# Optimization experiments

Hardware: AMD Instinct MI355X
Metric: run time of the kernel (lower is better)

The kernel has to match this reference:

```python
import jax, jax.numpy as jnp
import numpy as np

T, B, VD, KD, HD, OD = 64, 256, 64, 64, 512, 4


def setup_inputs() -> dict:
    key = jax.random.key(0)
    ks = jax.random.split(key, 20)
    s = 0.05
    p = {}
    p["images"] = jax.random.normal(ks[0], (T, B, 3, 32, 32), jnp.float32)
    # encoder: Conv(3->32,k4,s2) ReLU Conv(32->64,k4,s2) ReLU Conv(64->64,k4,s2) Flatten Linear(256->VD)
    p["conv1_w"] = jax.random.normal(ks[1], (32, 3, 4, 4), jnp.float32) * s
    p["conv1_b"] = jnp.zeros((32,), jnp.float32)
    p["conv2_w"] = jax.random.normal(ks[2], (64, 32, 4, 4), jnp.float32) * s
    p["conv2_b"] = jnp.zeros((64,), jnp.float32)
    p["conv3_w"] = jax.random.normal(ks[3], (64, 64, 4, 4), jnp.float32) * s
    p["conv3_b"] = jnp.zeros((64,), jnp.float32)
    p["enc_w"] = jax.random.normal(ks[4], (VD, 256), jnp.float32) * s
    p["enc_b"] = jnp.zeros((VD,), jnp.float32)
    # LSTMCell(key_dim+1 -> hidden_dim), torch gate order i,f,g,o
    p["w_ih"] = jax.random.normal(ks[5], (4 * HD, KD + 1), jnp.float32) * s
    p["w_hh"] = jax.random.normal(ks[6], (4 * HD, HD), jnp.float32) * s
    p["b_ih"] = jnp.zeros((4 * HD,), jnp.float32)
    p["b_hh"] = jnp.zeros((4 * HD,), jnp.float32)
    p["out_w"] = jax.random.normal(ks[7], (OD, HD), jnp.float32) * s
    p["out_b"] = jnp.zeros((OD,), jnp.float32)
    p["gate_w"] = jax.random.normal(ks[8], (1, HD), jnp.float32) * s
    p["gate_b"] = jnp.zeros((1,), jnp.float32)
    p["key_w"] = jax.random.normal(ks[9], (KD, HD), jnp.float32) * s
    p["key_b"] = jnp.zeros((KD,), jnp.float32)
    p["conf_w"] = jax.random.normal(ks[10], (1, 1), jnp.float32)
    p["conf_b"] = jnp.zeros((1,), jnp.float32)
    return p


def reference(images, conv1_w, conv1_b, conv2_w, conv2_b, conv3_w, conv3_b,
              enc_w, enc_b, w_ih, w_hh, b_ih, b_hh, out_w, out_b,
              gate_w, gate_b, key_w, key_b, conf_w, conf_b):
    Tn, Bn = images.shape[0], images.shape[1]

    def conv(x, w, b, relu):
        y = jax.lax.conv_general_dilated(
            x, w, window_strides=(2, 2), padding='VALID',
            dimension_numbers=('NCHW', 'OIHW', 'NCHW'))
        y = y + b[None, :, None, None]
        return jax.nn.relu(y) if relu else y

    # Encode all timesteps at once (same math as per-step encoder calls).
    x = images.reshape((Tn * Bn, 3, 32, 32))
    x = conv(x, conv1_w, conv1_b, True)
    x = conv(x, conv2_w, conv2_b, True)
    x = conv(x, conv3_w, conv3_b, False)  # no ReLU after 3rd conv in Sequential
    z_all = (x.reshape((Tn * Bn, -1)) @ enc_w.T + enc_b).reshape((Tn, Bn, -1))

    def lstm(x, h, c):
        g = x @ w_ih.T + b_ih + h @ w_hh.T + b_hh
        i, f, gg, o = jnp.split(g, 4, axis=-1)
        c2 = jax.nn.sigmoid(f) * c + jax.nn.sigmoid(i) * jnp.tanh(gg)
        return jax.nn.sigmoid(o) * jnp.tanh(c2), c2

    HDn = w_hh.shape[1]
    KDn = key_w.shape[0]
    VDn = z_all.shape[-1]
    slots = jnp.arange(Tn)

    def step(carry, xs):
        hx, cx, kx, Mk, Mv = carry
        z, t = xs
        hx, cx = lstm(kx, hx, cx)
        y = hx @ out_w.T + out_b
        g = hx @ gate_w.T + gate_b          # (b,1)
        kw = hx @ key_w.T + key_b           # (b,KD)
        # content-addressed read over the (masked) growing memory
        sim = jnp.einsum('bnd,bd->bn', Mv, z)
        mask = (slots < t)[None, :]
        wk = jax.nn.softmax(jnp.where(mask, sim, -1e30), axis=-1)
        ck = jax.nn.sigmoid(sim[..., None] * conf_w[0, 0] + conf_b[0])  # (b,n,1)
        mem = jnp.concatenate([Mk, ck], axis=-1)                         # (b,n,KD+1)
        kx_att = jax.nn.sigmoid(g) * jnp.einsum('bn,bnd->bd', wk, mem)
        kx_new = jnp.where(t == 0, jnp.zeros_like(kx_att), kx_att)      # k0 at first step
        # gated write: append kw / z at slot t
        Mk = Mk.at[:, t, :].set(kw)
        Mv = Mv.at[:, t, :].set(z)
        return (hx, cx, kx_new, Mk, Mv), y

    init = (jnp.zeros((Bn, HDn), images.dtype),
            jnp.zeros((Bn, HDn), images.dtype),
            jnp.zeros((Bn, KDn + 1), images.dtype),
            jnp.zeros((Bn, Tn, KDn), images.dtype),
            jnp.zeros((Bn, Tn, VDn), images.dtype))
    _, ys = jax.lax.scan(step, init, (z_all, slots))
    return ys  # (T, B, output_dim)
```

## Files before the change

kernel.cpp:

```cpp
#include <hip/hip_runtime.h>
#include <math.h>


__device__ __forceinline__ float sigm(float x) { return 1.0f / (1.0f + expf(-x)); }

#define PREP_N (1187840 + 2048 + 1536 + 32768 + 65536 + 16384)
__global__ __launch_bounds__(256) void prep_kernel(
    const float* __restrict__ w_ih, const float* __restrict__ w_hh,
    const float* __restrict__ b_ih, const float* __restrict__ b_hh,
    const float* __restrict__ w1, const float* __restrict__ w2,
    const float* __restrict__ w3, const float* __restrict__ ew,
    float* __restrict__ WT, float* __restrict__ bsum,
    float* __restrict__ w1T, float* __restrict__ w2T,
    float* __restrict__ w3T, float* __restrict__ ewT)
{
  int i = blockIdx.x * 256 + threadIdx.x;
  if (i < 1187840) {
    const int r = i >> 11, c = i & 2047;
    float v;
    if (r < 65)       v = w_ih[(size_t)c * 65 + r];
    else if (r < 577) v = w_hh[(size_t)c * 512 + (r - 65)];
    else              v = 0.0f;
    WT[i] = v; return;
  }
  i -= 1187840;
  if (i < 2048) { bsum[i] = b_ih[i] + b_hh[i]; return; }
  i -= 2048;
  if (i < 1536) { const int r = i >> 5, oc = i & 31; w1T[i] = w1[oc * 48 + r]; return; }
  i -= 1536;
  if (i < 32768) { const int r = i >> 6, oc = i & 63; w2T[i] = w2[oc * 512 + r]; return; }
  i -= 32768;
  if (i < 65536) { const int r = i >> 6, oc = i & 63; w3T[i] = w3[oc * 1024 + r]; return; }
  i -= 65536;
  if (i < 16384) { const int k = i >> 6, d = i & 63; ewT[i] = ew[d * 256 + k]; return; }
}

#define ENT 192
__global__ __launch_bounds__(ENT) void encoder_kernel(
    const float* __restrict__ images,
    const float* __restrict__ w1T, const float* __restrict__ b1,
    const float* __restrict__ w2T, const float* __restrict__ b2,
    const float* __restrict__ w3T, const float* __restrict__ b3,
    const float* __restrict__ ewT, const float* __restrict__ eb,
    float* __restrict__ z_all)
{
  __shared__ __align__(16) float c1[7744];
  __shared__ __align__(16) float buf[3072];
  const int bid = blockIdx.x;
  const int tid = threadIdx.x;

  {
    const float4* src = (const float4*)(images + (size_t)bid * 3072);
    float4* dst = (float4*)buf;
    for (int i = tid; i < 768; i += ENT) dst[i] = src[i];
  }
  __syncthreads();

  for (int s = tid; s < 360; s += ENT) {
    const int ocg  = s & 7;
    const int pg   = s >> 3;
    const int row  = pg / 3;
    const int colg = pg - row * 3;
    const int ox0  = colg * 5;
    float acc[4][5];
    #pragma unroll
    for (int o = 0; o < 4; ++o) {
      const float bb = b1[ocg * 4 + o];
      #pragma unroll
      for (int p = 0; p < 5; ++p) acc[o][p] = bb;
    }
    #pragma unroll
    for (int ic = 0; ic < 3; ++ic) {
      #pragma unroll
      for (int ky = 0; ky < 4; ++ky) {
        const int y = 2 * row + ky;
        const float* ib = &buf[ic * 1024 + y * 32 + 2 * ox0];
        float v[12];
        #pragma unroll
        for (int i = 0; i < 6; ++i) { float2 t2 = *(const float2*)(ib + 2 * i); v[2*i] = t2.x; v[2*i+1] = t2.y; }
        float w_[4][4];
        #pragma unroll
        for (int kx = 0; kx < 4; ++kx)
          *(float4*)&w_[kx][0] = *(const float4*)(w1T + (ic * 16 + ky * 4 + kx) * 32 + ocg * 4);
        #pragma unroll
        for (int o = 0; o < 4; ++o)
          #pragma unroll
          for (int p = 0; p < 5; ++p)
            acc[o][p] += w_[0][o] * v[2*p] + w_[1][o] * v[2*p+1] + w_[2][o] * v[2*p+2] + w_[3][o] * v[2*p+3];
      }
    }
    #pragma unroll
    for (int o = 0; o < 4; ++o)
      #pragma unroll
      for (int p = 0; p < 5; ++p)
        c1[(ocg * 4 + o) * 242 + row * 16 + ox0 + p] = fmaxf(acc[o][p], 0.0f);
  }
  __syncthreads();

  {
    const int ocg = tid & 15;
    const int pg  = tid >> 4;
    const int row = pg >> 1;
    const int ox0 = (pg & 1) * 3;
    float acc[4][3];
    #pragma unroll
    for (int o = 0; o < 4; ++o) {
      const float bb = b2[ocg * 4 + o];
      acc[o][0] = bb; acc[o][1] = bb; acc[o][2] = bb;
    }
    for (int ic = 0; ic < 32; ++ic) {
      #pragma unroll
      for (int ky = 0; ky < 4; ++ky) {
        const int y = 2 * row + ky;
        const float* ib = &c1[ic * 242 + y * 16 + 2 * ox0];
        float v[8];
        #pragma unroll
        for (int i = 0; i < 4; ++i) { float2 t2 = *(const float2*)(ib + 2 * i); v[2*i] = t2.x; v[2*i+1] = t2.y; }
        float w_[4][4];
        #pragma unroll
        for (int kx = 0; kx < 4; ++kx)
          *(float4*)&w_[kx][0] = *(const float4*)(w2T + (ic * 16 + ky * 4 + kx) * 64 + ocg * 4);
        #pragma unroll
        for (int o = 0; o < 4; ++o)
          #pragma unroll
          for (int p = 0; p < 3; ++p)
            acc[o][p] += w_[0][o] * v[2*p] + w_[1][o] * v[2*p+1] + w_[2][o] * v[2*p+2] + w_[3][o] * v[2*p+3];
      }
    }
    __syncthreads();
    #pragma unroll
    for (int o = 0; o < 4; ++o)
      #pragma unroll
      for (int p = 0; p < 3; ++p)
        buf[(ocg * 4 + o) * 38 + row * 6 + ox0 + p] = fmaxf(acc[o][p], 0.0f);
  }
  __syncthreads();

  {
    const int oc = tid & 63;
    const int kc = tid >> 6;
    const int k0 = (kc * 256) / 3, k1 = ((kc + 1) * 256) / 3;
    float acc[4] = {0.f, 0.f, 0.f, 0.f};
    for (int it = k0; it < k1; ++it) {
      const int ic = it >> 2;
      const int ky = it & 3;
      float v[2][6];
      #pragma unroll
      for (int oy = 0; oy < 2; ++oy) {
        const float* ib = &buf[ic * 38 + (2 * oy + ky) * 6];
        #pragma unroll
        for (int i = 0; i < 3; ++i) { float2 t2 = *(const float2*)(ib + 2 * i); v[oy][2*i] = t2.x; v[oy][2*i+1] = t2.y; }
      }
      float w_[4];
      #pragma unroll
      for (int kx = 0; kx < 4; ++kx) w_[kx] = w3T[(ic * 16 + ky * 4 + kx) * 64 + oc];
      #pragma unroll
      for (int p = 0; p < 4; ++p) {
        const int oy = p >> 1, ox = p & 1;
        acc[p] += w_[0] * v[oy][2*ox] + w_[1] * v[oy][2*ox+1] + w_[2] * v[oy][2*ox+2] + w_[3] * v[oy][2*ox+3];
      }
    }
    #pragma unroll
    for (int p = 0; p < 4; ++p) c1[kc * 260 + p * 64 + oc] = acc[p];
  }
  __syncthreads();

  for (int o = tid; o < 256; o += ENT) {
    const int oc = o >> 2, p = o & 3;
    c1[1024 + o] = b3[oc] + c1[p * 64 + oc] + c1[260 + p * 64 + oc] + c1[520 + p * 64 + oc];
  }
  __syncthreads();

  {
    const int d  = tid & 63;
    const int kc = tid >> 6;
    const int k0 = (kc * 256) / 3, k1 = ((kc + 1) * 256) / 3;
    float s = 0.0f;
    for (int k = k0; k < k1; ++k) s += ewT[k * 64 + d] * c1[1024 + k];
    c1[1536 + kc * 64 + d] = s;
  }
  __syncthreads();
  if (tid < 64) {
    z_all[(size_t)bid * 64 + tid] = eb[tid] + c1[1536 + tid] + c1[1600 + tid] + c1[1664 + tid];
  }
}

__global__ __launch_bounds__(256) void gram_kernel(
    const float* __restrict__ z_all, float* __restrict__ z_gram)
{
  const int b = blockIdx.x;
  const int tid = threadIdx.x;
  __shared__ float zsb[64 * 65];
  for (int i = tid; i < 4096; i += 256) {
    const int tt = i >> 6, d = i & 63;
    zsb[tt * 65 + d] = z_all[((size_t)tt * 256 + b) * 64 + d];
  }
  __syncthreads();
  const int n = tid & 63, tg = tid >> 6;
  for (int tt = tg; tt < 64; tt += 4) {
    float s = 0.0f;
    #pragma unroll
    for (int d = 0; d < 64; ++d) s += zsb[tt * 65 + d] * zsb[n * 65 + d];
    z_gram[((size_t)b * 64 + tt) * 64 + n] = s;
  }
}

__global__ __launch_bounds__(256) void gates_partial_kernel(
    const float* __restrict__ XC, const float* __restrict__ WT,
    float* __restrict__ Gp, const int kchunk, const int klog)
{
  extern __shared__ float xs[];
  const int bx  = blockIdx.x;
  const int kc  = bx & ((1 << klog) - 1);
  const int jt  = bx >> klog;
  const int tid = threadIdx.x;
  const int tj  = tid & 63, tb = tid >> 6;
  const int k0  = kc * kchunk;
  const int b0  = blockIdx.y * 16;
  const int j0  = jt * 256 + tj * 4;

  const int NS = 16 * kchunk;
  for (int i = tid; i < NS; i += 256) {
    const int b = i / kchunk, k = i - b * kchunk;
    xs[b * kchunk + k] = XC[(size_t)(b0 + b) * 580 + k0 + k];
  }
  __syncthreads();

  float acc[4][4];
  #pragma unroll
  for (int bb = 0; bb < 4; ++bb)
    #pragma unroll
    for (int jj = 0; jj < 4; ++jj) acc[bb][jj] = 0.0f;

  const float* wp = WT + (size_t)k0 * 2048 + j0;
  const float* xp = xs + tb * 4 * kchunk;
  #pragma unroll 4
  for (int k = 0; k < kchunk; ++k) {
    const float4 w = *(const float4*)(wp + (size_t)k * 2048);
    #pragma unroll
    for (int bb = 0; bb < 4; ++bb) {
      const float xv = xp[bb * kchunk + k];
      acc[bb][0] += xv * w.x; acc[bb][1] += xv * w.y;
      acc[bb][2] += xv * w.z; acc[bb][3] += xv * w.w;
    }
  }
  #pragma unroll
  for (int bb = 0; bb < 4; ++bb) {
    float4 r; r.x = acc[bb][0]; r.y = acc[bb][1]; r.z = acc[bb][2]; r.w = acc[bb][3];
    *(float4*)(Gp + ((size_t)kc * 256 + b0 + tb * 4 + bb) * 2048 + j0) = r;
  }
}

__global__ __launch_bounds__(256) void step_fused_kernel(
    const int t, const int kcn,
    const float* __restrict__ Gp, const float* __restrict__ bsum,
    float* __restrict__ C, const float* __restrict__ z_gram,
    float* __restrict__ MkT, float* __restrict__ XC, float* __restrict__ out,
    const float* __restrict__ out_w, const float* __restrict__ out_b,
    const float* __restrict__ gate_w, const float* __restrict__ gate_b,
    const float* __restrict__ key_w, const float* __restrict__ key_b,
    const float* __restrict__ conf_w, const float* __restrict__ conf_b)
{
  const int b   = blockIdx.x;
  const int tid = threadIdx.x;
  __shared__ __align__(16) float hs[512];
  __shared__ __align__(16) float wks[64];
  __shared__ __align__(16) float psum[256];
  __shared__ float sgv, kx64v;

  for (int jj = tid; jj < 512; jj += 256) {
    float gv[4];
    #pragma unroll
    for (int g = 0; g < 4; ++g) {
      float s = bsum[g * 512 + jj];
      for (int kc = 0; kc < kcn; ++kc)
        s += Gp[((size_t)kc * 256 + b) * 2048 + g * 512 + jj];
      gv[g] = s;
    }
    const size_t cidx = (size_t)b * 512 + jj;
    const float c2v = sigm(gv[1]) * C[cidx] + sigm(gv[0]) * tanhf(gv[2]);
    C[cidx] = c2v;
    const float h = sigm(gv[3]) * tanhf(c2v);
    hs[jj] = h;
    XC[(size_t)b * 580 + 65 + jj] = h;
  }
  __syncthreads();

  const int wv = tid >> 6, lane = tid & 63;
  for (int d = wv; d < 69; d += 4) {
    const float* row = (d < 64) ? (key_w + (size_t)d * 512)
                     : (d < 68) ? (out_w + (size_t)(d - 64) * 512)
                                : gate_w;
    float a = 0.0f;
    #pragma unroll
    for (int k = 0; k < 8; ++k) a += hs[lane + k * 64] * row[lane + k * 64];
    #pragma unroll
    for (int m = 32; m > 0; m >>= 1) a += __shfl_xor(a, m);
    if (lane == 0) {
      if (d < 64)      MkT[(size_t)b * 4096 + d * 64 + t] = a + key_b[d];
      else if (d < 68) out[(size_t)t * 1024 + b * 4 + (d - 64)] = a + out_b[d - 64];
      else             sgv = sigm(a + gate_b[0]);
    }
  }
  __syncthreads();

  if (t == 0) {
    if (tid < 65) XC[(size_t)b * 580 + tid] = 0.0f;
    return;
  }

  if (tid < 64) {
    const int n = tid;
    const float sim = z_gram[((size_t)b * 64 + t) * 64 + n];
    const bool valid = (n < t);
    float mx = valid ? sim : -3.0e38f;
    #pragma unroll
    for (int m = 32; m > 0; m >>= 1) mx = fmaxf(mx, __shfl_xor(mx, m));
    const float p = valid ? expf(sim - mx) : 0.0f;
    float sum = p;
    #pragma unroll
    for (int m = 32; m > 0; m >>= 1) sum += __shfl_xor(sum, m);
    const float wk = p / sum;
    wks[n] = wk;
    float kc = wk * sigm(sim * conf_w[0] + conf_b[0]);
    #pragma unroll
    for (int m = 32; m > 0; m >>= 1) kc += __shfl_xor(kc, m);
    if (n == 0) kx64v = kc;
  }
  __syncthreads();

  {
    const int d = tid >> 2, q = tid & 3;
    const float* mr = MkT + (size_t)b * 4096 + d * 64 + q * 16;
    const float* wr = wks + q * 16;
    float a = 0.0f;
    #pragma unroll
    for (int i = 0; i < 4; ++i) {
      const float4 m4 = *(const float4*)(mr + 4 * i);
      const float4 w4 = *(const float4*)(wr + 4 * i);
      a += m4.x * w4.x + m4.y * w4.y + m4.z * w4.z + m4.w * w4.w;
    }
    psum[tid] = a;
  }
  __syncthreads();
  if (tid < 64) {
    XC[(size_t)b * 580 + tid] = sgv * (psum[tid * 4] + psum[tid * 4 + 1] + psum[tid * 4 + 2] + psum[tid * 4 + 3]);
  } else if (tid == 64) {
    XC[(size_t)b * 580 + 64] = sgv * kx64v;
  }
}

extern "C" void kernel_launch(void* const* d_in, const int* in_sizes, int n_in,
                              void* d_out, int out_size, void* d_ws, size_t ws_size,
                              hipStream_t stream) {
  const float* images = (const float*)d_in[0];
  const float* w1     = (const float*)d_in[1];
  const float* b1     = (const float*)d_in[2];
  const float* w2     = (const float*)d_in[3];
  const float* b2     = (const float*)d_in[4];
  const float* w3     = (const float*)d_in[5];
  const float* b3     = (const float*)d_in[6];
  const float* ew     = (const float*)d_in[7];
  const float* eb     = (const float*)d_in[8];
  const float* w_ih   = (const float*)d_in[9];
  const float* w_hh   = (const float*)d_in[10];
  const float* b_ih   = (const float*)d_in[11];
  const float* b_hh   = (const float*)d_in[12];
  const float* out_w  = (const float*)d_in[13];
  const float* out_b  = (const float*)d_in[14];
  const float* gate_w = (const float*)d_in[15];
  const float* gate_b = (const float*)d_in[16];
  const float* key_w  = (const float*)d_in[17];
  const float* key_b  = (const float*)d_in[18];
  const float* conf_w = (const float*)d_in[19];
  const float* conf_b = (const float*)d_in[20];
  float* out = (float*)d_out;
  float* ws  = (float*)d_ws;

  float* WT     = ws;
  float* bsum   = ws + 1187840;
  float* w1T    = ws + 1189888;
  float* w2T    = ws + 1191424;
  float* w3T    = ws + 1224192;
  float* ewT    = ws + 1289728;
  float* z_all  = ws + 1306112;
  float* MkT    = ws + 2354688;
  float* C      = ws + 3403264;
  float* XC     = ws + 3534336;
  float* z_gram = ws + 3682816;
  float* Gp     = ws + 4731392;

  int kcn = 4, klog = 2, kchunk = 145;
  if (ws_size < (4731392ull + 4ull * 524288ull) * 4ull) { kcn = 2; klog = 1; kchunk = 290; }
  if (ws_size < (4731392ull + 2ull * 524288ull) * 4ull) { kcn = 1; klog = 0; kchunk = 580; }

  hipMemsetAsync(C,  0, 131072 * sizeof(float), stream);
  hipMemsetAsync(XC, 0, 148480 * sizeof(float), stream);

  prep_kernel<<<(PREP_N + 255) / 256, 256, 0, stream>>>(
      w_ih, w_hh, b_ih, b_hh, w1, w2, w3, ew, WT, bsum, w1T, w2T, w3T, ewT);

  encoder_kernel<<<16384, ENT, 0, stream>>>(images, w1T, b1, w2T, b2, w3T, b3, ewT, eb, z_all);

  gram_kernel<<<256, 256, 0, stream>>>(z_all, z_gram);

  const size_t lds_stage = (size_t)16 * kchunk * sizeof(float);
  for (int t = 0; t < 64; ++t) {
    gates_partial_kernel<<<dim3(8 * kcn, 16), 256, lds_stage, stream>>>(
        XC, WT, Gp, kchunk, klog);
    step_fused_kernel<<<256, 256, 0, stream>>>(
        t, kcn, Gp, bsum, C, z_gram, MkT, XC, out,
        out_w, out_b, gate_w, gate_b, key_w, key_b, conf_w, conf_b);
  }
}
```

Before: 4.132 ms.

## Fuse recurrent scan into one cooperative kernel and split encoder conv1

The 64-step recurrence, which used two kernel launches per step, now runs as a single cooperative persistent kernel that uses grid-wide syncs between the gate GEMM phase and the per-batch update phase. When workspace allows, the encoder is also split into a conv1 kernel that writes its activations to global memory and a second kernel that runs the remaining layers. This targets per-step launch overhead and encoder occupancy, which the large LDS use of the fused encoder had limited. In exchange it adds grid.sync costs, global round trips for conv1 outputs, and depends on the cooperative grid fitting co-resident on the device.

```diff
diff --git a/kernel.cpp b/kernel.cpp
--- a/kernel.cpp
+++ b/kernel.cpp
@@ -1,5 +1,8 @@
 #include <hip/hip_runtime.h>
+#include <hip/hip_cooperative_groups.h>
 #include <math.h>
+
+namespace cg = cooperative_groups;
 
 
 __device__ __forceinline__ float sigm(float x) { return 1.0f / (1.0f + expf(-x)); }
@@ -36,6 +39,169 @@
 }
 
 #define ENT 192
+__global__ __launch_bounds__(ENT) void conv1_kernel(
+    const float* __restrict__ images,
+    const float* __restrict__ w1T, const float* __restrict__ b1,
+    float* __restrict__ c1g, const int s0)
+{
+  __shared__ __align__(16) float buf[3072];
+  const int bid = blockIdx.x;
+  const int tid = threadIdx.x;
+  {
+    const float4* src = (const float4*)(images + (size_t)(s0 + bid) * 3072);
+    float4* dst = (float4*)buf;
+    for (int i = tid; i < 768; i += ENT) dst[i] = src[i];
+  }
+  __syncthreads();
+
+  float* outp = c1g + (size_t)bid * 7680;
+  for (int s = tid; s < 360; s += ENT) {
+    const int ocg  = s & 7;
+    const int pg   = s >> 3;
+    const int row  = pg / 3;
+    const int colg = pg - row * 3;
+    const int ox0  = colg * 5;
+    float acc[4][5];
+    #pragma unroll
+    for (int o = 0; o < 4; ++o) {
+      const float bb = b1[ocg * 4 + o];
+      #pragma unroll
+      for (int p = 0; p < 5; ++p) acc[o][p] = bb;
+    }
+    #pragma unroll
+    for (int ic = 0; ic < 3; ++ic) {
+      #pragma unroll
+      for (int ky = 0; ky < 4; ++ky) {
+        const int y = 2 * row + ky;
+        const float* ib = &buf[ic * 1024 + y * 32 + 2 * ox0];
+        float v[12];
+        #pragma unroll
+        for (int i = 0; i < 6; ++i) { float2 t2 = *(const float2*)(ib + 2 * i); v[2*i] = t2.x; v[2*i+1] = t2.y; }
+        float w_[4][4];
+        #pragma unroll
+        for (int kx = 0; kx < 4; ++kx)
+          *(float4*)&w_[kx][0] = *(const float4*)(w1T + (ic * 16 + ky * 4 + kx) * 32 + ocg * 4);
+        #pragma unroll
+        for (int o = 0; o < 4; ++o)
+          #pragma unroll
+          for (int p = 0; p < 5; ++p)
+            acc[o][p] += w_[0][o] * v[2*p] + w_[1][o] * v[2*p+1] + w_[2][o] * v[2*p+2] + w_[3][o] * v[2*p+3];
+      }
+    }
+    #pragma unroll
+    for (int o = 0; o < 4; ++o)
+      #pragma unroll
+      for (int p = 0; p < 5; ++p)
+        outp[(ocg * 4 + o) * 240 + row * 16 + ox0 + p] = fmaxf(acc[o][p], 0.0f);
+  }
+}
+
+__global__ __launch_bounds__(ENT) void enc2_kernel(
+    const float* __restrict__ c1g,
+    const float* __restrict__ w2T, const float* __restrict__ b2,
+    const float* __restrict__ w3T, const float* __restrict__ b3,
+    const float* __restrict__ ewT, const float* __restrict__ eb,
+    float* __restrict__ z_all, const int s0)
+{
+  __shared__ __align__(16) float c1[7680];
+  __shared__ __align__(16) float buf[2432];
+  const int bid = blockIdx.x;
+  const int tid = threadIdx.x;
+
+  {
+    const float4* src = (const float4*)(c1g + (size_t)bid * 7680);
+    float4* dst = (float4*)c1;
+    for (int i = tid; i < 1920; i += ENT) dst[i] = src[i];
+  }
+  __syncthreads();
+
+  {
+    const int ocg = tid & 15;
+    const int pg  = tid >> 4;
+    const int row = pg >> 1;
+    const int ox0 = (pg & 1) * 3;
+    float acc[4][3];
+    #pragma unroll
+    for (int o = 0; o < 4; ++o) {
+      const float bb = b2[ocg * 4 + o];
+      acc[o][0] = bb; acc[o][1] = bb; acc[o][2] = bb;
+    }
+    for (int ic = 0; ic < 32; ++ic) {
+      #pragma unroll
+      for (int ky = 0; ky < 4; ++ky) {
+        const int y = 2 * row + ky;
+        const float* ib = &c1[ic * 240 + y * 16 + 2 * ox0];
+        float v[8];
+        #pragma unroll
+        for (int i = 0; i < 4; ++i) { float2 t2 = *(const float2*)(ib + 2 * i); v[2*i] = t2.x; v[2*i+1] = t2.y; }
+        float w_[4][4];
+        #pragma unroll
+        for (int kx = 0; kx < 4; ++kx)
+          *(float4*)&w_[kx][0] = *(const float4*)(w2T + (ic * 16 + ky * 4 + kx) * 64 + ocg * 4);
+        #pragma unroll
+        for (int o = 0; o < 4; ++o)
+          #pragma unroll
+          for (int p = 0; p < 3; ++p)
+            acc[o][p] += w_[0][o] * v[2*p] + w_[1][o] * v[2*p+1] + w_[2][o] * v[2*p+2] + w_[3][o] * v[2*p+3];
+      }
+    }
+    #pragma unroll
+    for (int o = 0; o < 4; ++o)
+      #pragma unroll
+      for (int p = 0; p < 3; ++p)
+        buf[(ocg * 4 + o) * 38 + row * 6 + ox0 + p] = fmaxf(acc[o][p], 0.0f);
+  }
+  __syncthreads();
+
+  {
+    const int oc = tid & 63;
+    const int kc = tid >> 6;
+    const int k0 = (kc * 256) / 3, k1 = ((kc + 1) * 256) / 3;
+    float acc[4] = {0.f, 0.f, 0.f, 0.f};
+    for (int it = k0; it < k1; ++it) {
+      const int ic = it >> 2;
+      const int ky = it & 3;
+      float v[2][6];
+      #pragma unroll
+      for (int oy = 0; oy < 2; ++oy) {
+        const float* ib = &buf[ic * 38 + (2 * oy + ky) * 6];
+        #pragma unroll
+        for (int i = 0; i < 3; ++i) { float2 t2 = *(const float2*)(ib + 2 * i); v[oy][2*i] = t2.x; v[oy][2*i+1] = t2.y; }
+      }
+      float w_[4];
+      #pragma unroll
+      for (int kx = 0; kx < 4; ++kx) w_[kx] = w3T[(ic * 16 + ky * 4 + kx) * 64 + oc];
+      #pragma unroll
+      for (int p = 0; p < 4; ++p) {
+        const int oy = p >> 1, ox = p & 1;
+        acc[p] += w_[0] * v[oy][2*ox] + w_[1] * v[oy][2*ox+1] + w_[2] * v[oy][2*ox+2] + w_[3] * v[oy][2*ox+3];
+      }
+    }
+    #pragma unroll
+    for (int p = 0; p < 4; ++p) c1[kc * 260 + p * 64 + oc] = acc[p];
+  }
+  __syncthreads();
+
+  for (int o = tid; o < 256; o += ENT) {
+    const int oc = o >> 2, p = o & 3;
+    c1[1024 + o] = b3[oc] + c1[p * 64 + oc] + c1[260 + p * 64 + oc] + c1[520 + p * 64 + oc];
+  }
+  __syncthreads();
+
+  {
+    const int d  = tid & 63;
+    const int kc = tid >> 6;
+    const int k0 = (kc * 256) / 3, k1 = ((kc + 1) * 256) / 3;
+    float s = 0.0f;
+    for (int k = k0; k < k1; ++k) s += ewT[k * 64 + d] * c1[1024 + k];
+    c1[1536 + kc * 64 + d] = s;
+  }
+  __syncthreads();
+  if (tid < 64) {
+    z_all[(size_t)(s0 + bid) * 64 + tid] = eb[tid] + c1[1536 + tid] + c1[1600 + tid] + c1[1664 + tid];
+  }
+}
+
 __global__ __launch_bounds__(ENT) void encoder_kernel(
     const float* __restrict__ images,
     const float* __restrict__ w1T, const float* __restrict__ b1,
@@ -48,14 +214,12 @@
   __shared__ __align__(16) float buf[3072];
   const int bid = blockIdx.x;
   const int tid = threadIdx.x;
-
   {
     const float4* src = (const float4*)(images + (size_t)bid * 3072);
     float4* dst = (float4*)buf;
     for (int i = tid; i < 768; i += ENT) dst[i] = src[i];
   }
   __syncthreads();
-
   for (int s = tid; s < 360; s += ENT) {
     const int ocg  = s & 7;
     const int pg   = s >> 3;
@@ -96,7 +260,6 @@
         c1[(ocg * 4 + o) * 242 + row * 16 + ox0 + p] = fmaxf(acc[o][p], 0.0f);
   }
   __syncthreads();
-
   {
     const int ocg = tid & 15;
     const int pg  = tid >> 4;
@@ -135,7 +298,6 @@
         buf[(ocg * 4 + o) * 38 + row * 6 + ox0 + p] = fmaxf(acc[o][p], 0.0f);
   }
   __syncthreads();
-
   {
     const int oc = tid & 63;
     const int kc = tid >> 6;
@@ -164,13 +326,11 @@
     for (int p = 0; p < 4; ++p) c1[kc * 260 + p * 64 + oc] = acc[p];
   }
   __syncthreads();
-
   for (int o = tid; o < 256; o += ENT) {
     const int oc = o >> 2, p = o & 3;
     c1[1024 + o] = b3[oc] + c1[p * 64 + oc] + c1[260 + p * 64 + oc] + c1[520 + p * 64 + oc];
   }
   __syncthreads();
-
   {
     const int d  = tid & 63;
     const int kc = tid >> 6;
@@ -205,148 +365,148 @@
   }
 }
 
-__global__ __launch_bounds__(256) void gates_partial_kernel(
-    const float* __restrict__ XC, const float* __restrict__ WT,
-    float* __restrict__ Gp, const int kchunk, const int klog)
-{
-  extern __shared__ float xs[];
-  const int bx  = blockIdx.x;
-  const int kc  = bx & ((1 << klog) - 1);
-  const int jt  = bx >> klog;
-  const int tid = threadIdx.x;
-  const int tj  = tid & 63, tb = tid >> 6;
-  const int k0  = kc * kchunk;
-  const int b0  = blockIdx.y * 16;
-  const int j0  = jt * 256 + tj * 4;
-
-  const int NS = 16 * kchunk;
-  for (int i = tid; i < NS; i += 256) {
-    const int b = i / kchunk, k = i - b * kchunk;
-    xs[b * kchunk + k] = XC[(size_t)(b0 + b) * 580 + k0 + k];
-  }
-  __syncthreads();
-
-  float acc[4][4];
-  #pragma unroll
-  for (int bb = 0; bb < 4; ++bb)
-    #pragma unroll
-    for (int jj = 0; jj < 4; ++jj) acc[bb][jj] = 0.0f;
-
-  const float* wp = WT + (size_t)k0 * 2048 + j0;
-  const float* xp = xs + tb * 4 * kchunk;
-  #pragma unroll 4
-  for (int k = 0; k < kchunk; ++k) {
-    const float4 w = *(const float4*)(wp + (size_t)k * 2048);
-    #pragma unroll
-    for (int bb = 0; bb < 4; ++bb) {
-      const float xv = xp[bb * kchunk + k];
-      acc[bb][0] += xv * w.x; acc[bb][1] += xv * w.y;
-      acc[bb][2] += xv * w.z; acc[bb][3] += xv * w.w;
-    }
-  }
-  #pragma unroll
-  for (int bb = 0; bb < 4; ++bb) {
-    float4 r; r.x = acc[bb][0]; r.y = acc[bb][1]; r.z = acc[bb][2]; r.w = acc[bb][3];
-    *(float4*)(Gp + ((size_t)kc * 256 + b0 + tb * 4 + bb) * 2048 + j0) = r;
-  }
-}
-
-__global__ __launch_bounds__(256) void step_fused_kernel(
-    const int t, const int kcn,
-    const float* __restrict__ Gp, const float* __restrict__ bsum,
+__global__ __launch_bounds__(256, 2) void scan_coop_kernel(
+    const float* __restrict__ WT, const float* __restrict__ bsum,
     float* __restrict__ C, const float* __restrict__ z_gram,
-    float* __restrict__ MkT, float* __restrict__ XC, float* __restrict__ out,
+    float* __restrict__ MkT, float* __restrict__ XC, float* __restrict__ Gp,
+    float* __restrict__ o_ptr,
     const float* __restrict__ out_w, const float* __restrict__ out_b,
     const float* __restrict__ gate_w, const float* __restrict__ gate_b,
     const float* __restrict__ key_w, const float* __restrict__ key_b,
-    const float* __restrict__ conf_w, const float* __restrict__ conf_b)
+    const float* __restrict__ conf_w, const float* __restrict__ conf_b,
+    const int kcn, const int klog, const int kchunk)
 {
-  const int b   = blockIdx.x;
+  cg::grid_group grid = cg::this_grid();
+  __shared__ __align__(16) float smem[16 * 580];
+
   const int tid = threadIdx.x;
-  __shared__ __align__(16) float hs[512];
-  __shared__ __align__(16) float wks[64];
-  __shared__ __align__(16) float psum[256];
-  __shared__ float sgv, kx64v;
-
-  for (int jj = tid; jj < 512; jj += 256) {
-    float gv[4];
-    #pragma unroll
-    for (int g = 0; g < 4; ++g) {
-      float s = bsum[g * 512 + jj];
-      for (int kc = 0; kc < kcn; ++kc)
-        s += Gp[((size_t)kc * 256 + b) * 2048 + g * 512 + jj];
-      gv[g] = s;
-    }
-    const size_t cidx = (size_t)b * 512 + jj;
-    const float c2v = sigm(gv[1]) * C[cidx] + sigm(gv[0]) * tanhf(gv[2]);
-    C[cidx] = c2v;
-    const float h = sigm(gv[3]) * tanhf(c2v);
-    hs[jj] = h;
-    XC[(size_t)b * 580 + 65 + jj] = h;
-  }
-  __syncthreads();
-
-  const int wv = tid >> 6, lane = tid & 63;
-  for (int d = wv; d < 69; d += 4) {
-    const float* row = (d < 64) ? (key_w + (size_t)d * 512)
-                     : (d < 68) ? (out_w + (size_t)(d - 64) * 512)
-                                : gate_w;
-    float a = 0.0f;
-    #pragma unroll
-    for (int k = 0; k < 8; ++k) a += hs[lane + k * 64] * row[lane + k * 64];
-    #pragma unroll
-    for (int m = 32; m > 0; m >>= 1) a += __shfl_xor(a, m);
-    if (lane == 0) {
-      if (d < 64)      MkT[(size_t)b * 4096 + d * 64 + t] = a + key_b[d];
-      else if (d < 68) out[(size_t)t * 1024 + b * 4 + (d - 64)] = a + out_b[d - 64];
-      else             sgv = sigm(a + gate_b[0]);
-    }
-  }
-  __syncthreads();
-
-  if (t == 0) {
-    if (tid < 65) XC[(size_t)b * 580 + tid] = 0.0f;
-    return;
-  }
-
-  if (tid < 64) {
-    const int n = tid;
-    const float sim = z_gram[((size_t)b * 64 + t) * 64 + n];
-    const bool valid = (n < t);
-    float mx = valid ? sim : -3.0e38f;
-    #pragma unroll
-    for (int m = 32; m > 0; m >>= 1) mx = fmaxf(mx, __shfl_xor(mx, m));
-    const float p = valid ? expf(sim - mx) : 0.0f;
-    float sum = p;
-    #pragma unroll
-    for (int m = 32; m > 0; m >>= 1) sum += __shfl_xor(sum, m);
-    const float wk = p / sum;
-    wks[n] = wk;
-    float kc = wk * sigm(sim * conf_w[0] + conf_b[0]);
-    #pragma unroll
-    for (int m = 32; m > 0; m >>= 1) kc += __shfl_xor(kc, m);
-    if (n == 0) kx64v = kc;
-  }
-  __syncthreads();
-
-  {
-    const int d = tid >> 2, q = tid & 3;
-    const float* mr = MkT + (size_t)b * 4096 + d * 64 + q * 16;
-    const float* wr = wks + q * 16;
-    float a = 0.0f;
-    #pragma unroll
-    for (int i = 0; i < 4; ++i) {
-      const float4 m4 = *(const float4*)(mr + 4 * i);
-      const float4 w4 = *(const float4*)(wr + 4 * i);
-      a += m4.x * w4.x + m4.y * w4.y + m4.z * w4.z + m4.w * w4.w;
-    }
-    psum[tid] = a;
-  }
-  __syncthreads();
-  if (tid < 64) {
-    XC[(size_t)b * 580 + tid] = sgv * (psum[tid * 4] + psum[tid * 4 + 1] + psum[tid * 4 + 2] + psum[tid * 4 + 3]);
-  } else if (tid == 64) {
-    XC[(size_t)b * 580 + 64] = sgv * kx64v;
+  const int gid = blockIdx.x;
+  const int jt  = gid & 7;
+  const int kc  = (gid >> 3) & (kcn - 1);
+  const int bt  = gid >> (3 + klog);
+  const int tj  = tid & 63, tb = tid >> 6;
+  const int k0  = kc * kchunk;
+  const int b0  = bt * 16;
+  const int j0  = jt * 256 + tj * 4;
+  const int NS  = 16 * kchunk;
+
+  for (int t = 0; t < 64; ++t) {
+    for (int i = tid; i < NS; i += 256) {
+      const int b = i / kchunk, k = i - b * kchunk;
+      smem[b * kchunk + k] = XC[(size_t)(b0 + b) * 580 + k0 + k];
+    }
+    __syncthreads();
+    {
+      float acc[4][4];
+      #pragma unroll
+      for (int bb = 0; bb < 4; ++bb) { acc[bb][0]=0.f; acc[bb][1]=0.f; acc[bb][2]=0.f; acc[bb][3]=0.f; }
+      const float* wp = WT + (size_t)k0 * 2048 + j0;
+      const float* xp = smem + tb * 4 * kchunk;
+      #pragma unroll 4
+      for (int k = 0; k < kchunk; ++k) {
+        const float4 w = *(const float4*)(wp + (size_t)k * 2048);
+        #pragma unroll
+        for (int bb = 0; bb < 4; ++bb) {
+          const float xv = xp[bb * kchunk + k];
+          acc[bb][0] += xv * w.x; acc[bb][1] += xv * w.y;
+          acc[bb][2] += xv * w.z; acc[bb][3] += xv * w.w;
+        }
+      }
+      #pragma unroll
+      for (int bb = 0; bb < 4; ++bb) {
+        float4 r; r.x = acc[bb][0]; r.y = acc[bb][1]; r.z = acc[bb][2]; r.w = acc[bb][3];
+        *(float4*)(Gp + ((size_t)kc * 256 + b0 + tb * 4 + bb) * 2048 + j0) = r;
+      }
+    }
+    grid.sync();
+
+    for (int b = gid; b < 256; b += gridDim.x) {
+      float* hs   = smem;
+      float* wks  = smem + 512;
+      float* psum = smem + 576;
+      float* sgp  = smem + 832;
+      float* kxp  = smem + 833;
+      __syncthreads();
+      for (int jj = tid; jj < 512; jj += 256) {
+        float gv[4];
+        #pragma unroll
+        for (int g = 0; g < 4; ++g) {
+          float s = bsum[g * 512 + jj];
+          for (int kc2 = 0; kc2 < kcn; ++kc2)
+            s += Gp[((size_t)kc2 * 256 + b) * 2048 + g * 512 + jj];
+          gv[g] = s;
+        }
+        const size_t cidx = (size_t)b * 512 + jj;
+        const float c2v = sigm(gv[1]) * C[cidx] + sigm(gv[0]) * tanhf(gv[2]);
+        C[cidx] = c2v;
+        const float h = sigm(gv[3]) * tanhf(c2v);
+        hs[jj] = h;
+        XC[(size_t)b * 580 + 65 + jj] = h;
+      }
+      __syncthreads();
+
+      const int wv = tid >> 6, lane = tid & 63;
+      for (int d = wv; d < 69; d += 4) {
+        const float* row = (d < 64) ? (key_w + (size_t)d * 512)
+                         : (d < 68) ? (out_w + (size_t)(d - 64) * 512)
+                                    : gate_w;
+        float a = 0.0f;
+        #pragma unroll
+        for (int k = 0; k < 8; ++k) a += hs[lane + k * 64] * row[lane + k * 64];
+        #pragma unroll
+        for (int m = 32; m > 0; m >>= 1) a += __shfl_xor(a, m);
+        if (lane == 0) {
+          if (d < 64)      MkT[(size_t)b * 4096 + d * 64 + t] = a + key_b[d];
+          else if (d < 68) o_ptr[(size_t)t * 1024 + b * 4 + (d - 64)] = a + out_b[d - 64];
+          else             *sgp = sigm(a + gate_b[0]);
+        }
+      }
+      __syncthreads();
+
+      if (t == 0) {
+        if (tid < 65) XC[(size_t)b * 580 + tid] = 0.0f;
+      } else {
+        if (tid < 64) {
+          const int n = tid;
+          const float sim = z_gram[((size_t)b * 64 + t) * 64 + n];
+          const bool valid = (n < t);
+          float mx = valid ? sim : -3.0e38f;
+          #pragma unroll
+          for (int m = 32; m > 0; m >>= 1) mx = fmaxf(mx, __shfl_xor(mx, m));
+          const float p = valid ? expf(sim - mx) : 0.0f;
+          float sum = p;
+          #pragma unroll
+          for (int m = 32; m > 0; m >>= 1) sum += __shfl_xor(sum, m);
+          const float wk = p / sum;
+          wks[n] = wk;
+          float kcv = wk * sigm(sim * conf_w[0] + conf_b[0]);
+          #pragma unroll
+          for (int m = 32; m > 0; m >>= 1) kcv += __shfl_xor(kcv, m);
+          if (n == 0) *kxp = kcv;
+        }
+        __syncthreads();
+        {
+          const int d = tid >> 2, q = tid & 3;
+          const float* mr = MkT + (size_t)b * 4096 + d * 64 + q * 16;
+          const float* wr = wks + q * 16;
+          float a = 0.0f;
+          #pragma unroll
+          for (int i = 0; i < 4; ++i) {
+            const float4 m4 = *(const float4*)(mr + 4 * i);
+            const float4 w4 = *(const float4*)(wr + 4 * i);
+            a += m4.x * w4.x + m4.y * w4.y + m4.z * w4.z + m4.w * w4.w;
+          }
+          psum[tid] = a;
+        }
+        __syncthreads();
+        if (tid < 64) {
+          XC[(size_t)b * 580 + tid] = (*sgp) * (psum[tid * 4] + psum[tid * 4 + 1] + psum[tid * 4 + 2] + psum[tid * 4 + 3]);
+        } else if (tid == 64) {
+          XC[(size_t)b * 580 + 64] = (*sgp) * (*kxp);
+        }
+      }
+    }
+    grid.sync();
   }
 }
 
@@ -374,8 +534,8 @@
   const float* key_b  = (const float*)d_in[18];
   const float* conf_w = (const float*)d_in[19];
   const float* conf_b = (const float*)d_in[20];
-  float* out = (float*)d_out;
-  float* ws  = (float*)d_ws;
+  float* o_ptr = (float*)d_out;
+  float* ws    = (float*)d_ws;
 
   float* WT     = ws;
   float* bsum   = ws + 1187840;
@@ -394,22 +554,35 @@
   if (ws_size < (4731392ull + 4ull * 524288ull) * 4ull) { kcn = 2; klog = 1; kchunk = 290; }
   if (ws_size < (4731392ull + 2ull * 524288ull) * 4ull) { kcn = 1; klog = 0; kchunk = 580; }
 
+  const size_t baseF  = 4731392ull + (size_t)kcn * 524288ull;
+  float* c1g          = ws + baseF;
+  const size_t availF = (ws_size / 4 > baseF) ? (ws_size / 4 - baseF) : 0;
+  long chunkL = (long)(availF / 7680ull);
+  int chunk = (chunkL > 16384) ? 16384 : (int)chunkL;
+
   hipMemsetAsync(C,  0, 131072 * sizeof(float), stream);
   hipMemsetAsync(XC, 0, 148480 * sizeof(float), stream);
 
   prep_kernel<<<(PREP_N + 255) / 256, 256, 0, stream>>>(
       w_ih, w_hh, b_ih, b_hh, w1, w2, w3, ew, WT, bsum, w1T, w2T, w3T, ewT);
 
-  encoder_kernel<<<16384, ENT, 0, stream>>>(images, w1T, b1, w2T, b2, w3T, b3, ewT, eb, z_all);
+  if (chunk >= 2048) {
+    for (int s0 = 0; s0 < 16384; s0 += chunk) {
+      const int n = (16384 - s0 < chunk) ? (16384 - s0) : chunk;
+      conv1_kernel<<<n, ENT, 0, stream>>>(images, w1T, b1, c1g, s0);
+      enc2_kernel<<<n, ENT, 0, stream>>>(c1g, w2T, b2, w3T, b3, ewT, eb, z_all, s0);
+    }
+  } else {
+    encoder_kernel<<<16384, ENT, 0, stream>>>(images, w1T, b1, w2T, b2, w3T, b3, ewT, eb, z_all);
+  }
 
   gram_kernel<<<256, 256, 0, stream>>>(z_all, z_gram);
 
-  const size_t lds_stage = (size_t)16 * kchunk * sizeof(float);
-  for (int t = 0; t < 64; ++t) {
-    gates_partial_kernel<<<dim3(8 * kcn, 16), 256, lds_stage, stream>>>(
-        XC, WT, Gp, kchunk, klog);
-    step_fused_kernel<<<256, 256, 0, stream>>>(
-        t, kcn, Gp, bsum, C, z_gram, MkT, XC, out,
-        out_w, out_b, gate_w, gate_b, key_w, key_b, conf_w, conf_b);
-  }
-}
+  void* args[] = { (void*)&WT, (void*)&bsum, (void*)&C, (void*)&z_gram,
+                   (void*)&MkT, (void*)&XC, (void*)&Gp, (void*)&o_ptr,
+                   (void*)&out_w, (void*)&out_b, (void*)&gate_w, (void*)&gate_b,
+                   (void*)&key_w, (void*)&key_b, (void*)&conf_w, (void*)&conf_b,
+                   (void*)&kcn, (void*)&klog, (void*)&kchunk };
+  hipLaunchCooperativeKernel((void*)scan_coop_kernel, dim3(128 * kcn), dim3(256),
+                             args, 0, stream);
+}
```

Result: slower. 11.30 ms (+173.5%).
